# Kernel tuning notes

Hardware: AMD Instinct MI355X
Metric: run time of the kernel (lower is better)

The kernel has to match this reference:

```python
import jax, jax.numpy as jnp
import numpy as np

LAMBDA = 1.0  # lambda_ from __init__


def _exact_edt(targets):
    """Exact Euclidean distance transform of (1 - targets), i.e. distance from
    each pixel to the nearest pixel where targets == 1. Matches
    scipy.ndimage.distance_transform_edt(1 - targets) per batch sample.
    targets: [B, H, W] int (binary). Returns float32 [B, H, W].
    Separable algorithm:
      G(h, w)   = min_{h': seed(h',w)} |h - h'|        (1D pass along H, via cummax/cummin)
      D(h, w)^2 = min_{w'} (w - w')^2 + G(h, w')^2     (min over columns, broadcast)
    """
    B, H, W = targets.shape
    seed = targets > 0  # [B,H,W]
    h_idx = jnp.arange(H, dtype=jnp.float32)[None, :, None]  # [1,H,1]
    # distance to nearest seed above (running max of seed row-indices)
    last_seed = jax.lax.cummax(jnp.where(seed, h_idx, -jnp.inf), axis=1)
    d_up = h_idx - last_seed
    # distance to nearest seed below (reversed running min of seed row-indices)
    next_seed = jnp.flip(jax.lax.cummin(jnp.flip(jnp.where(seed, h_idx, jnp.inf), 1), axis=1), 1)
    d_dn = next_seed - h_idx
    g2 = jnp.square(jnp.minimum(d_up, d_dn))  # [B,H,W] squared 1D distance (inf if column empty)
    w_idx = jnp.arange(W, dtype=jnp.float32)
    off2 = jnp.square(w_idx[:, None] - w_idx[None, :])  # [W_out, W_in]
    # D2[b,h,wo] = min_wi g2[b,h,wi] + off2[wo,wi]; intermediate [B,H,W,W]
    d2 = jnp.min(g2[:, :, None, :] + off2[None, None, :, :], axis=-1)
    return jnp.sqrt(d2)


def setup_inputs() -> dict:
    key = jax.random.key(0)
    k1, k2 = jax.random.split(key)
    B, H, W = 4, 320, 320
    logits = jax.random.normal(k1, (B, H, W), dtype=jnp.float32)
    targets = jax.random.randint(k2, (B, H, W), 0, 2, dtype=jnp.int32)
    return {"logits": logits, "targets": targets}


def reference(logits, targets):
    probs = jax.nn.sigmoid(logits)
    distance_maps = _exact_edt(targets)  # constant w.r.t. logits (cpu/numpy round-trip in original)
    return (probs * distance_maps).mean() + LAMBDA * (1.0 - probs).mean()
```

## Files before the change

kernel.cpp:

```cpp
#include <hip/hip_runtime.h>
#include <math.h>

#define B_ 4
#define H_ 320
#define W_ 320
#define N_TOTAL (B_ * H_ * W_)
#define BLOCK 256
#define NBLK (N_TOTAL / BLOCK)

__global__ __launch_bounds__(BLOCK) void fused_edt_loss(
        const float* __restrict__ logits,
        const int* __restrict__ tgt,
        double* __restrict__ partial ) {
    int idx = blockIdx.x * BLOCK + threadIdx.x;
    int b = idx / (H_ * W_);
    int rem = idx - b * (H_ * W_);
    int h = rem / W_;
    int w = rem - h * W_;
    const int* __restrict__ img = tgt + b * (H_ * W_);

    int best2 = 0x7fffffff;
    if (img[h * W_ + w] > 0) best2 = 0;

    for (int r = 1; r < H_ + W_; ++r) {
        int r2 = r * r;
        if (r2 >= best2) break;
        int hlo = h - r, hhi = h + r;
        int wlo = w - r, whi = w + r;
        int wl = wlo > 0 ? wlo : 0;
        int wr = whi < (W_ - 1) ? whi : (W_ - 1);
        if (hlo >= 0) {
            const int* rowp = img + hlo * W_;
            for (int ww = wl; ww <= wr; ++ww)
                if (rowp[ww] > 0) {
                    int dw = ww - w;
                    int d2 = r2 + dw * dw;
                    best2 = d2 < best2 ? d2 : best2;
                }
        }
        if (hhi < H_) {
            const int* rowp = img + hhi * W_;
            for (int ww = wl; ww <= wr; ++ww)
                if (rowp[ww] > 0) {
                    int dw = ww - w;
                    int d2 = r2 + dw * dw;
                    best2 = d2 < best2 ? d2 : best2;
                }
        }
        int hl = (hlo + 1) > 0 ? (hlo + 1) : 0;
        int hr = (hhi - 1) < (H_ - 1) ? (hhi - 1) : (H_ - 1);
        if (wlo >= 0) {
            for (int hh = hl; hh <= hr; ++hh)
                if (img[hh * W_ + wlo] > 0) {
                    int dh = hh - h;
                    int d2 = dh * dh + r2;
                    best2 = d2 < best2 ? d2 : best2;
                }
        }
        if (whi < W_) {
            for (int hh = hl; hh <= hr; ++hh)
                if (img[hh * W_ + whi] > 0) {
                    int dh = hh - h;
                    int d2 = dh * dh + r2;
                    best2 = d2 < best2 ? d2 : best2;
                }
        }
    }

    float d = sqrtf((float)best2);
    float x = logits[idx];
    float p = 1.0f / (1.0f + expf(-x));
    double v1 = (double)(p * d);
    double v2 = (double)(1.0f - p);

    for (int off = 32; off > 0; off >>= 1) {
        v1 += __shfl_down(v1, off, 64);
        v2 += __shfl_down(v2, off, 64);
    }
    __shared__ double s1[BLOCK / 64], s2[BLOCK / 64];
    int wave = threadIdx.x >> 6;
    if ((threadIdx.x & 63) == 0) { s1[wave] = v1; s2[wave] = v2; }
    __syncthreads();
    if (threadIdx.x == 0) {
        partial[2 * blockIdx.x]     = s1[0] + s1[1] + s1[2] + s1[3];
        partial[2 * blockIdx.x + 1] = s2[0] + s2[1] + s2[2] + s2[3];
    }
}

__global__ __launch_bounds__(256) void final_reduce(
        const double* __restrict__ partial, float* __restrict__ out) {
    double v1 = 0.0, v2 = 0.0;
    for (int i = threadIdx.x; i < NBLK; i += 256) {
        v1 += partial[2 * i];
        v2 += partial[2 * i + 1];
    }
    for (int off = 32; off > 0; off >>= 1) {
        v1 += __shfl_down(v1, off, 64);
        v2 += __shfl_down(v2, off, 64);
    }
    __shared__ double s1[4], s2[4];
    int wave = threadIdx.x >> 6;
    if ((threadIdx.x & 63) == 0) { s1[wave] = v1; s2[wave] = v2; }
    __syncthreads();
    if (threadIdx.x == 0) {
        double a = s1[0] + s1[1] + s1[2] + s1[3];
        double c = s2[0] + s2[1] + s2[2] + s2[3];
        out[0] = (float)((a + c) / (double)N_TOTAL);
    }
}

extern "C" void kernel_launch(void* const* d_in, const int* in_sizes, int n_in,
                              void* d_out, int out_size, void* d_ws, size_t ws_size,
                              hipStream_t stream) {
    const float* logits = (const float*)d_in[0];
    const int* targets  = (const int*)d_in[1];
    float* out = (float*)d_out;
    double* partial = (double*)d_ws;

    fused_edt_loss<<<NBLK, BLOCK, 0, stream>>>(logits, targets, partial);
    final_reduce<<<1, 256, 0, stream>>>(partial, out);
}
```

Baseline: 65.12 us.

## Bit-pack target rows into shared memory and search nearest seed with ctz/clz

Each block now handles 4 image rows. It stages a halo of 12 rows as 64-bit ballot bitmasks in shared memory, then finds the nearest seed per row window with count-trailing/leading-zero operations over a ±32 column window. If no seed lies within the halo radius, it falls back to the original global-memory ring scan. This replaces the per-pixel ring scan over global memory with a few shared-memory bit operations, at the cost of a fixed halo staging step per block and divergent fallback paths.

```diff
diff --git a/kernel.cpp b/kernel.cpp
--- a/kernel.cpp
+++ b/kernel.cpp
@@ -5,23 +5,17 @@
 #define H_ 320
 #define W_ 320
 #define N_TOTAL (B_ * H_ * W_)
+#define ROWS 4
+#define HALO 4
+#define RSTAGE (ROWS + 2 * HALO)
+#define GROUPS (RSTAGE * 5)
+#define BLOCKS_PER_B (H_ / ROWS)
+#define NBLK (B_ * BLOCKS_PER_B)
 #define BLOCK 256
-#define NBLK (N_TOTAL / BLOCK)
 
-__global__ __launch_bounds__(BLOCK) void fused_edt_loss(
-        const float* __restrict__ logits,
-        const int* __restrict__ tgt,
-        double* __restrict__ partial ) {
-    int idx = blockIdx.x * BLOCK + threadIdx.x;
-    int b = idx / (H_ * W_);
-    int rem = idx - b * (H_ * W_);
-    int h = rem / W_;
-    int w = rem - h * W_;
-    const int* __restrict__ img = tgt + b * (H_ * W_);
-
+__device__ int fallback_ring_scan(const int* __restrict__ img, int h, int w) {
     int best2 = 0x7fffffff;
-    if (img[h * W_ + w] > 0) best2 = 0;
-
+    if (img[h * W_ + w] > 0) return 0;
     for (int r = 1; r < H_ + W_; ++r) {
         int r2 = r * r;
         if (r2 >= best2) break;
@@ -32,58 +26,101 @@
         if (hlo >= 0) {
             const int* rowp = img + hlo * W_;
             for (int ww = wl; ww <= wr; ++ww)
-                if (rowp[ww] > 0) {
-                    int dw = ww - w;
-                    int d2 = r2 + dw * dw;
-                    best2 = d2 < best2 ? d2 : best2;
-                }
+                if (rowp[ww] > 0) { int dw = ww - w; int d2 = r2 + dw * dw; best2 = d2 < best2 ? d2 : best2; }
         }
         if (hhi < H_) {
             const int* rowp = img + hhi * W_;
             for (int ww = wl; ww <= wr; ++ww)
-                if (rowp[ww] > 0) {
-                    int dw = ww - w;
-                    int d2 = r2 + dw * dw;
-                    best2 = d2 < best2 ? d2 : best2;
-                }
+                if (rowp[ww] > 0) { int dw = ww - w; int d2 = r2 + dw * dw; best2 = d2 < best2 ? d2 : best2; }
         }
         int hl = (hlo + 1) > 0 ? (hlo + 1) : 0;
         int hr = (hhi - 1) < (H_ - 1) ? (hhi - 1) : (H_ - 1);
         if (wlo >= 0) {
             for (int hh = hl; hh <= hr; ++hh)
-                if (img[hh * W_ + wlo] > 0) {
-                    int dh = hh - h;
-                    int d2 = dh * dh + r2;
-                    best2 = d2 < best2 ? d2 : best2;
-                }
+                if (img[hh * W_ + wlo] > 0) { int dh = hh - h; int d2 = dh * dh + r2; best2 = d2 < best2 ? d2 : best2; }
         }
         if (whi < W_) {
             for (int hh = hl; hh <= hr; ++hh)
-                if (img[hh * W_ + whi] > 0) {
-                    int dh = hh - h;
-                    int d2 = dh * dh + r2;
-                    best2 = d2 < best2 ? d2 : best2;
-                }
+                if (img[hh * W_ + whi] > 0) { int dh = hh - h; int d2 = dh * dh + r2; best2 = d2 < best2 ? d2 : best2; }
         }
     }
+    return best2;
+}
 
-    float d = sqrtf((float)best2);
-    float x = logits[idx];
-    float p = 1.0f / (1.0f + expf(-x));
-    double v1 = (double)(p * d);
-    double v2 = (double)(1.0f - p);
+__device__ __forceinline__ int nearest_dw(const unsigned long long* __restrict__ row, int w) {
+    int s = w + 32;
+    int word = s >> 6, sh = s & 63;
+    unsigned long long lo = row[word];
+    unsigned long long win = sh ? ((lo >> sh) | (row[word + 1] << (64 - sh))) : lo;
+    int dw = 64;
+    unsigned long long rw = win >> 32;
+    unsigned long long lw = win << 32;
+    if (rw) dw = __builtin_ctzll(rw);
+    if (lw) { int dl = __builtin_clzll(lw) + 1; if (dl < dw) dw = dl; }
+    return dw;
+}
+
+__global__ __launch_bounds__(BLOCK) void fused_edt_loss(
+        const float* __restrict__ logits,
+        const int* __restrict__ tgt,
+        double* __restrict__ partial ) {
+    __shared__ unsigned long long smrow[RSTAGE][8];
+
+    int bid = blockIdx.x;
+    int b = bid / BLOCKS_PER_B;
+    int g = bid - b * BLOCKS_PER_B;
+    int r0 = g * ROWS;
+    const int* __restrict__ img = tgt + b * (H_ * W_);
+    int t = threadIdx.x;
+    int wv = t >> 6, lane = t & 63;
+
+    if (t < RSTAGE) { smrow[t][0] = 0; smrow[t][6] = 0; smrow[t][7] = 0; }
+    for (int gg = wv; gg < GROUPS; gg += 4) {
+        int rr = gg / 5, wd = gg - rr * 5;
+        int gr = r0 - HALO + rr;
+        bool p = false;
+        if (gr >= 0 && gr < H_) p = img[gr * W_ + wd * 64 + lane] > 0;
+        unsigned long long m = __ballot(p);
+        if (lane == 0) smrow[rr][1 + wd] = m;
+    }
+    __syncthreads();
+
+    int sr = HALO + wv;
+    int gh = r0 + wv;
+    const float* lrow = logits + (b * H_ + gh) * W_;
+    double v1 = 0.0, v2 = 0.0;
+
+    for (int k = 0; k < 5; ++k) {
+        int w = lane + (k << 6);
+        int dw0 = nearest_dw(smrow[sr], w);
+        int best2 = (dw0 < 64) ? dw0 * dw0 : 0x3fffffff;
+        for (int dh = 1; dh <= HALO; ++dh) {
+            int dh2 = dh * dh;
+            if (dh2 >= best2) break;
+            int du = nearest_dw(smrow[sr - dh], w);
+            if (du < 64) { int c = dh2 + du * du; if (c < best2) best2 = c; }
+            int dd = nearest_dw(smrow[sr + dh], w);
+            if (dd < 64) { int c = dh2 + dd * dd; if (c < best2) best2 = c; }
+        }
+        if (best2 > (HALO + 1) * (HALO + 1)) best2 = fallback_ring_scan(img, gh, w);
+
+        float dist = sqrtf((float)best2);
+        float x = lrow[w];
+        float p = 1.0f / (1.0f + expf(-x));
+        v1 += (double)(p * dist);
+        v2 += (double)(1.0f - p);
+    }
 
     for (int off = 32; off > 0; off >>= 1) {
         v1 += __shfl_down(v1, off, 64);
         v2 += __shfl_down(v2, off, 64);
     }
     __shared__ double s1[BLOCK / 64], s2[BLOCK / 64];
-    int wave = threadIdx.x >> 6;
-    if ((threadIdx.x & 63) == 0) { s1[wave] = v1; s2[wave] = v2; }
+    if (lane == 0) { s1[wv] = v1; s2[wv] = v2; }
     __syncthreads();
-    if (threadIdx.x == 0) {
-        partial[2 * blockIdx.x]     = s1[0] + s1[1] + s1[2] + s1[3];
-        partial[2 * blockIdx.x + 1] = s2[0] + s2[1] + s2[2] + s2[3];
+    if (t == 0) {
+        partial[2 * bid]     = s1[0] + s1[1] + s1[2] + s1[3];
+        partial[2 * bid + 1] = s2[0] + s2[1] + s2[2] + s2[3];
     }
 }
 
```

Result: slower. 67.21 us (+3.2%).
